# Kernel tuning notes

Measured on AMD Instinct MI355X. Metric: run time of the kernel, lower is better.

The kernel has to match this reference:

```python
import jax, jax.numpy as jnp
import numpy as np

DROPOUT = 0.1      # ban radius in normalized coords
INVALID = -2.0     # PositionGetter.INVALID sentinel
EPS = 1e-08


def setup_inputs() -> dict:
    key = jax.random.key(0)
    k1, k2, k3 = jax.random.split(key, 3)
    B, C, T, D = 64, 275, 3000, 2
    x = jax.random.normal(k1, (B, C, T), dtype=jnp.float32)
    positions = jax.random.uniform(k2, (B, C, D), dtype=jnp.float32)
    # row 0: the ban center applied to x; rows 1..100: Monte-Carlo test centers
    centers = jax.random.uniform(k3, (101, D), dtype=jnp.float32)
    return {"x": x, "positions": positions, "centers": centers}


def reference(x, positions, centers):
    # valid_mask: channel is valid unless all coords equal the INVALID sentinel
    valid = ~jnp.all(positions == INVALID, axis=-1)          # [B, C] bool
    x = x * valid[..., None].astype(x.dtype)
    # distances from every channel position to every center, all at once
    # centers: [N, D], positions: [B, C, D] -> dist: [N, B, C]
    diff = positions[None, :, :, :] - centers[:, None, None, :]
    dist = jnp.linalg.norm(diff, axis=-1)                    # [N, B, C]
    kept_all = (dist > DROPOUT) | (~valid)[None]             # [N, B, C] bool
    # apply the actual ban (first center)
    x = x * kept_all[0][..., None].astype(x.dtype)
    # Monte-Carlo keep probability over the remaining 100 centers
    prob_kept = jnp.mean(kept_all[1:].astype(x.dtype), axis=0)  # [B, C]
    return x / (prob_kept[..., None] + EPS)
```

## Files before the change

### kernel.cpp

```cpp
#include <hip/hip_runtime.h>
#include <math.h>


typedef float f32x4 __attribute__((ext_vector_type(4)));

__global__ __launch_bounds__(256) void ChannelDropout_14851996910142_kernel(
    const float* __restrict__ x,
    const float* __restrict__ pos,
    const float* __restrict__ centers,
    float* __restrict__ out,
    int ncenters, int tlen)
{
    const int row  = blockIdx.x;
    const int tid  = threadIdx.x;
    const int lane = tid & 63;

    const size_t base = (size_t)row * (size_t)tlen;
    const int t4 = tlen >> 2;
    const f32x4* __restrict__ xr   = (const f32x4*)(x + base);
    f32x4* __restrict__       orow = (f32x4*)(out + base);

    const int i0 = tid, i1 = tid + 256, i2 = tid + 512;
    const bool p0 = i0 < t4, p1 = i1 < t4, p2 = i2 < t4;
    f32x4 v0 = {}, v1 = {}, v2 = {};
    if (p0) v0 = xr[i0];
    if (p1) v1 = xr[i1];
    if (p2) v2 = xr[i2];

    const float px = pos[2 * row];
    const float py = pos[2 * row + 1];
    const bool valid = !(px == -2.0f && py == -2.0f);

    float cnt = 0.0f;
    for (int c = 1 + lane; c < ncenters; c += 64) {
        const float dx = px - centers[2 * c];
        const float dy = py - centers[2 * c + 1];
        const float d2 = __fadd_rn(__fmul_rn(dx, dx), __fmul_rn(dy, dy));
        cnt += (sqrtf(d2) > 0.1f) ? 1.0f : 0.0f;
    }
    #pragma unroll
    for (int off = 32; off > 0; off >>= 1)
        cnt += __shfl_xor(cnt, off, 64);

    const float dx0 = px - centers[0];
    const float dy0 = py - centers[1];
    const float d02 = __fadd_rn(__fmul_rn(dx0, dx0), __fmul_rn(dy0, dy0));
    const bool kept0 = sqrtf(d02) > 0.1f;
    const float prob = cnt / (float)(ncenters - 1);
    const float s = (valid && kept0) ? (1.0f / (prob + 1e-8f)) : 0.0f;

    if (p0) __builtin_nontemporal_store(v0 * s, orow + i0);
    if (p1) __builtin_nontemporal_store(v1 * s, orow + i1);
    if (p2) __builtin_nontemporal_store(v2 * s, orow + i2);

    for (int i = tid + 768; i < t4; i += 256) {
        f32x4 v = xr[i];
        __builtin_nontemporal_store(v * s, orow + i);
    }
    for (int i = (t4 << 2) + tid; i < tlen; i += 256) {
        out[base + i] = x[base + i] * s;
    }
}

extern "C" void kernel_launch(void* const* d_in, const int* in_sizes, int n_in,
                              void* d_out, int out_size, void* d_ws, size_t ws_size,
                              hipStream_t stream) {
    const float* x       = (const float*)d_in[0];
    const float* pos     = (const float*)d_in[1];
    const float* centers = (const float*)d_in[2];
    float* out = (float*)d_out;

    const int rows     = in_sizes[1] / 2;
    const int tlen     = in_sizes[0] / rows;
    const int ncenters = in_sizes[2] / 2;

    ChannelDropout_14851996910142_kernel<<<rows, 256, 0, stream>>>(
        x, pos, centers, out, ncenters, tlen);
}
```

Before: 358.3 us.

## Split scale computation into separate kernel and use persistent grid-stride apply kernel

Computes the per-row scale in a small kernel, one wavefront per row, and writes it to workspace. A second kernel with 2048 blocks grid-strides over rows to apply the scale with vectorized nontemporal stores. This takes the center-distance computation and its dependency chain off the memory-streaming path and cuts the number of block launches, at the cost of an extra kernel launch and a workspace round-trip. It also drops the early loads of x that used to be issued before the scale was computed, and keeps a fused fallback for when no workspace is available.

```diff
diff --git a/kernel.cpp b/kernel.cpp
--- a/kernel.cpp
+++ b/kernel.cpp
@@ -4,31 +4,18 @@
 
 typedef float f32x4 __attribute__((ext_vector_type(4)));
 
-__global__ __launch_bounds__(256) void ChannelDropout_14851996910142_kernel(
-    const float* __restrict__ x,
+__global__ __launch_bounds__(256) void ChannelDropout_scales_kernel(
     const float* __restrict__ pos,
     const float* __restrict__ centers,
-    float* __restrict__ out,
-    int ncenters, int tlen)
+    float* __restrict__ scale,
+    int rows, int ncenters)
 {
-    const int row  = blockIdx.x;
-    const int tid  = threadIdx.x;
-    const int lane = tid & 63;
+    const int wid  = (int)((blockIdx.x * 256u + threadIdx.x) >> 6);
+    const int lane = threadIdx.x & 63;
+    if (wid >= rows) return;
 
-    const size_t base = (size_t)row * (size_t)tlen;
-    const int t4 = tlen >> 2;
-    const f32x4* __restrict__ xr   = (const f32x4*)(x + base);
-    f32x4* __restrict__       orow = (f32x4*)(out + base);
-
-    const int i0 = tid, i1 = tid + 256, i2 = tid + 512;
-    const bool p0 = i0 < t4, p1 = i1 < t4, p2 = i2 < t4;
-    f32x4 v0 = {}, v1 = {}, v2 = {};
-    if (p0) v0 = xr[i0];
-    if (p1) v1 = xr[i1];
-    if (p2) v2 = xr[i2];
-
-    const float px = pos[2 * row];
-    const float py = pos[2 * row + 1];
+    const float px = pos[2 * wid];
+    const float py = pos[2 * wid + 1];
     const bool valid = !(px == -2.0f && py == -2.0f);
 
     float cnt = 0.0f;
@@ -42,24 +29,82 @@
     for (int off = 32; off > 0; off >>= 1)
         cnt += __shfl_xor(cnt, off, 64);
 
+    if (lane == 0) {
+        const float dx0 = px - centers[0];
+        const float dy0 = py - centers[1];
+        const float d02 = __fadd_rn(__fmul_rn(dx0, dx0), __fmul_rn(dy0, dy0));
+        const bool kept0 = sqrtf(d02) > 0.1f;
+        const int denom = (ncenters > 1) ? (ncenters - 1) : 1;
+        const float prob = cnt / (float)denom;
+        scale[wid] = (valid && kept0) ? (1.0f / (prob + 1e-8f)) : 0.0f;
+    }
+}
+
+__global__ __launch_bounds__(256) void ChannelDropout_apply_kernel(
+    const float* __restrict__ x,
+    const float* __restrict__ scale,
+    float* __restrict__ out,
+    int rows, int tlen)
+{
+    const int tid = threadIdx.x;
+    const int t4  = tlen >> 2;
+    for (int row = blockIdx.x; row < rows; row += gridDim.x) {
+        const float s = scale[row];
+        const size_t base = (size_t)row * (size_t)tlen;
+        const f32x4* __restrict__ xr   = (const f32x4*)(x + base);
+        f32x4* __restrict__       orow = (f32x4*)(out + base);
+        for (int i = tid; i < t4; i += 256) {
+            f32x4 v = xr[i];
+            __builtin_nontemporal_store(v * s, orow + i);
+        }
+        for (int i = (t4 << 2) + tid; i < tlen; i += 256) {
+            out[base + i] = x[base + i] * s;
+        }
+    }
+}
+
+__global__ __launch_bounds__(256) void ChannelDropout_fused_kernel(
+    const float* __restrict__ x,
+    const float* __restrict__ pos,
+    const float* __restrict__ centers,
+    float* __restrict__ out,
+    int ncenters, int tlen)
+{
+    const int row  = blockIdx.x;
+    const int tid  = threadIdx.x;
+    const int lane = tid & 63;
+
+    const float px = pos[2 * row];
+    const float py = pos[2 * row + 1];
+    const bool valid = !(px == -2.0f && py == -2.0f);
+    float cnt = 0.0f;
+    for (int c = 1 + lane; c < ncenters; c += 64) {
+        const float dx = px - centers[2 * c];
+        const float dy = py - centers[2 * c + 1];
+        const float d2 = __fadd_rn(__fmul_rn(dx, dx), __fmul_rn(dy, dy));
+        cnt += (sqrtf(d2) > 0.1f) ? 1.0f : 0.0f;
+    }
+    #pragma unroll
+    for (int off = 32; off > 0; off >>= 1)
+        cnt += __shfl_xor(cnt, off, 64);
     const float dx0 = px - centers[0];
     const float dy0 = py - centers[1];
     const float d02 = __fadd_rn(__fmul_rn(dx0, dx0), __fmul_rn(dy0, dy0));
     const bool kept0 = sqrtf(d02) > 0.1f;
-    const float prob = cnt / (float)(ncenters - 1);
+    const int denom = (ncenters > 1) ? (ncenters - 1) : 1;
+    const float prob = cnt / (float)denom;
     const float s = (valid && kept0) ? (1.0f / (prob + 1e-8f)) : 0.0f;
 
-    if (p0) __builtin_nontemporal_store(v0 * s, orow + i0);
-    if (p1) __builtin_nontemporal_store(v1 * s, orow + i1);
-    if (p2) __builtin_nontemporal_store(v2 * s, orow + i2);
-
-    for (int i = tid + 768; i < t4; i += 256) {
+    const size_t base = (size_t)row * (size_t)tlen;
+    const int t4 = tlen >> 2;
+    const f32x4* __restrict__ xr   = (const f32x4*)(x + base);
+    f32x4* __restrict__       orow = (f32x4*)(out + base);
+    for (int i = tid; i < t4; i += 256) {
         f32x4 v = xr[i];
         __builtin_nontemporal_store(v * s, orow + i);
     }
-    for (int i = (t4 << 2) + tid; i < tlen; i += 256) {
+    for (int i = (t4 << 2) + tid; i < tlen; i += 256)
         out[base + i] = x[base + i] * s;
-    }
 }
 
 extern "C" void kernel_launch(void* const* d_in, const int* in_sizes, int n_in,
@@ -74,6 +119,16 @@
     const int tlen     = in_sizes[0] / rows;
     const int ncenters = in_sizes[2] / 2;
 
-    ChannelDropout_14851996910142_kernel<<<rows, 256, 0, stream>>>(
-        x, pos, centers, out, ncenters, tlen);
+    if (d_ws != nullptr && ws_size >= (size_t)rows * sizeof(float)) {
+        float* scale = (float*)d_ws;
+        const int ablocks = (rows + 3) / 4;
+        ChannelDropout_scales_kernel<<<ablocks, 256, 0, stream>>>(
+            pos, centers, scale, rows, ncenters);
+        const int bblocks = 2048;
+        ChannelDropout_apply_kernel<<<bblocks, 256, 0, stream>>>(
+            x, scale, out, rows, tlen);
+    } else {
+        ChannelDropout_fused_kernel<<<rows, 256, 0, stream>>>(
+            x, pos, centers, out, ncenters, tlen);
+    }
 }
```

Result: slower. 374.9 us (+4.6%).
